# Kernel tuning notes

Measured on AMD Instinct MI355X. Metric: run time of the kernel, lower is better.

The kernel has to match this reference:

```python
import jax, jax.numpy as jnp
import numpy as np

# NF4 codebook (bitsandbytes quant_type='nf4'), 16 fixed quantile values
NF4 = jnp.array([
    -1.0, -0.6961928009986877, -0.5250730514526367, -0.39491748809814453,
    -0.28444138169288635, -0.18477343022823334, -0.09105003625154495, 0.0,
    0.07958029955625534, 0.16093020141124725, 0.24611230194568634,
    0.33791524171829224, 0.44070982933044434, 0.5626170039176941,
    0.7229568362236023, 1.0], dtype=jnp.float32)
BLK = 64  # bnb default blocksize for nf4


def dequant_nf4(codes, absmax):
    # codes: [out, in] int codes in [0,16); absmax: [out, in//BLK] blockwise scale
    out_f, in_f = codes.shape
    w = NF4[codes].reshape(out_f, in_f // BLK, BLK) * absmax[:, :, None]
    return w.reshape(out_f, in_f)


def setup_inputs() -> dict:
    key = jax.random.key(0)
    ks = jax.random.split(key, 7)
    hd, m, T = 4096, 14336, 2048
    x = jax.random.normal(ks[0], (T, hd), dtype=jnp.float32)
    gate_codes = jax.random.randint(ks[1], (m, hd), 0, 16, dtype=jnp.int32)
    gate_absmax = jax.random.uniform(ks[2], (m, hd // BLK), dtype=jnp.float32) * 0.05
    up_codes = jax.random.randint(ks[3], (m, hd), 0, 16, dtype=jnp.int32)
    up_absmax = jax.random.uniform(ks[4], (m, hd // BLK), dtype=jnp.float32) * 0.05
    down_codes = jax.random.randint(ks[5], (hd, m), 0, 16, dtype=jnp.int32)
    down_absmax = jax.random.uniform(ks[6], (hd, m // BLK), dtype=jnp.float32) * 0.05
    return {"x": x, "gate_codes": gate_codes, "gate_absmax": gate_absmax,
            "up_codes": up_codes, "up_absmax": up_absmax,
            "down_codes": down_codes, "down_absmax": down_absmax}


def reference(x, gate_codes, gate_absmax, up_codes, up_absmax, down_codes, down_absmax):
    # SwiGLU MLP: down( silu(gate(x)) * up(x) ), weights dequantized from nf4
    Wg = dequant_nf4(gate_codes, gate_absmax)   # [m, hd]
    Wu = dequant_nf4(up_codes, up_absmax)       # [m, hd]
    Wd = dequant_nf4(down_codes, down_absmax)   # [hd, m]
    g = x @ Wg.T                                # [T, m]
    h = jax.nn.silu(g) * (x @ Wu.T)             # [T, m]
    return h @ Wd.T                             # [T, hd]
```

## Files before the change

kernel.cpp:

```cpp
#include <hip/hip_runtime.h>
#include <hip/hip_bf16.h>
#include <cstdint>
#include <cstddef>

#define TDIM 2048
#define HDIM 4096
#define MDIM 14336

typedef __attribute__((ext_vector_type(8))) __bf16 bf16x8;
typedef __attribute__((ext_vector_type(4))) float f32x4;

__device__ __constant__ float NF4_LUT[16] = {
    -1.0f, -0.6961928009986877f, -0.5250730514526367f, -0.39491748809814453f,
    -0.28444138169288635f, -0.18477343022823334f, -0.09105003625154495f, 0.0f,
    0.07958029955625534f, 0.16093020141124725f, 0.24611230194568634f,
    0.33791524171829224f, 0.44070982933044434f, 0.5626170039176941f,
    0.7229568362236023f, 1.0f};

__device__ inline void g2l16(const void* g, void* l) {
  __builtin_amdgcn_global_load_lds(
      (const __attribute__((address_space(1))) unsigned int*)g,
      (__attribute__((address_space(3))) unsigned int*)l,
      16 , 0, 0);
}

__global__ __launch_bounds__(256) void f32_to_bf16_k(
    const float* __restrict__ in, __hip_bfloat16* __restrict__ out, int n8) {
  for (int i = blockIdx.x * 256 + threadIdx.x; i < n8; i += gridDim.x * 256) {
    const float4* p = (const float4*)(in + (size_t)i * 8);
    float4 a = p[0], b = p[1];
    union { __hip_bfloat16 h[8]; int4 v; } u;
    u.h[0] = __float2bfloat16(a.x);
    u.h[1] = __float2bfloat16(a.y);
    u.h[2] = __float2bfloat16(a.z);
    u.h[3] = __float2bfloat16(a.w);
    u.h[4] = __float2bfloat16(b.x);
    u.h[5] = __float2bfloat16(b.y);
    u.h[6] = __float2bfloat16(b.z);
    u.h[7] = __float2bfloat16(b.w);
    *(int4*)(out + (size_t)i * 8) = u.v;
  }
}

__global__ __launch_bounds__(256) void dequant_nf4_k(
    const int* __restrict__ codes, const float* __restrict__ absmax,
    __hip_bfloat16* __restrict__ W, int K) {
  __shared__ float lut[16];
  if (threadIdx.x < 16) lut[threadIdx.x] = NF4_LUT[threadIdx.x];
  __syncthreads();
  const int row = blockIdx.x;
  const int K8 = K >> 3;
  const size_t rbase = (size_t)row * K;
  for (int c8 = threadIdx.x; c8 < K8; c8 += 256) {
    const int col = c8 << 3;
    const float am = absmax[(size_t)row * (K >> 6) + (col >> 6)];
    const int4* cp = (const int4*)(codes + rbase + col);
    int4 ca = cp[0], cb = cp[1];
    union { __hip_bfloat16 h[8]; int4 v; } u;
    u.h[0] = __float2bfloat16(lut[ca.x & 15] * am);
    u.h[1] = __float2bfloat16(lut[ca.y & 15] * am);
    u.h[2] = __float2bfloat16(lut[ca.z & 15] * am);
    u.h[3] = __float2bfloat16(lut[ca.w & 15] * am);
    u.h[4] = __float2bfloat16(lut[cb.x & 15] * am);
    u.h[5] = __float2bfloat16(lut[cb.y & 15] * am);
    u.h[6] = __float2bfloat16(lut[cb.z & 15] * am);
    u.h[7] = __float2bfloat16(lut[cb.w & 15] * am);
    *(int4*)(W + rbase + col) = u.v;
  }
}

template <int EPI>
__global__ __launch_bounds__(256, 2) void gemm_nt_k(
    const __hip_bfloat16* __restrict__ A, const __hip_bfloat16* __restrict__ B,
    void* __restrict__ Cv, const __hip_bfloat16* __restrict__ Gin,
    int M, int N, int K) {
  __shared__ __align__(16) char sA[128 * 128];
  __shared__ __align__(16) char sB[128 * 128];

  const int tid = threadIdx.x;
  const int lane = tid & 63;
  const int wid = tid >> 6;

  const int nbn = N >> 7;
  const int nwg = (M >> 7) * nbn;
  const int cpx = nwg >> 3;
  const int bid = blockIdx.x;
  const int wg = (bid & 7) * cpx + (bid >> 3);
  const int bm = wg / nbn, bn = wg % nbn;

  const int srow = lane >> 3;
  const int scolb = ((lane & 7) ^ srow) << 4;
  const char* gA = (const char*)A +
      ((size_t)(bm * 128 + wid * 8 + srow) * K) * 2 + scolb;
  const char* gB = (const char*)B +
      ((size_t)(bn * 128 + wid * 8 + srow) * K) * 2 + scolb;
  const size_t cstep = (size_t)64 * K;
  char* lA = sA + wid * 1024;
  char* lB = sB + wid * 1024;

  const int wm = wid >> 1, wn = wid & 1;
  const int colsw = (((lane >> 4) << 4) ^ ((lane & 7) << 4));
  const int aoff = (wm * 64 + (lane & 15)) * 128 + colsw;
  const int boff = (wn * 64 + (lane & 15)) * 128 + colsw;

  f32x4 acc[4][4] = {};

  const int nk = K >> 6;
  for (int kt = 0; kt < nk; ++kt) {
    const char* pa = gA + (size_t)kt * 128;
    const char* pb = gB + (size_t)kt * 128;
#pragma unroll
    for (int c = 0; c < 4; ++c) {
      g2l16(pa + c * cstep, lA + c * 4096);
      g2l16(pb + c * cstep, lB + c * 4096);
    }
    __syncthreads();
#pragma unroll
    for (int ks = 0; ks < 2; ++ks) {
      bf16x8 af[4], bfr[4];
#pragma unroll
      for (int i = 0; i < 4; ++i) {
        af[i] = *(const bf16x8*)(sA + ((aoff + i * 2048) ^ (ks << 6)));
        bfr[i] = *(const bf16x8*)(sB + ((boff + i * 2048) ^ (ks << 6)));
      }
#pragma unroll
      for (int mi = 0; mi < 4; ++mi)
#pragma unroll
        for (int nj = 0; nj < 4; ++nj)
          acc[mi][nj] = __builtin_amdgcn_mfma_f32_16x16x32_bf16(
              af[mi], bfr[nj], acc[mi][nj], 0, 0, 0);
    }
    __syncthreads();
  }

  const int row0 = bm * 128 + wm * 64 + ((lane >> 4) << 2);
  const int col0 = bn * 128 + wn * 64 + (lane & 15);
#pragma unroll
  for (int mi = 0; mi < 4; ++mi) {
#pragma unroll
    for (int nj = 0; nj < 4; ++nj) {
#pragma unroll
      for (int r = 0; r < 4; ++r) {
        const size_t idx =
            (size_t)(row0 + mi * 16 + r) * N + (col0 + nj * 16);
        const float v = acc[mi][nj][r];
        if (EPI == 0) {
          ((__hip_bfloat16*)Cv)[idx] = __float2bfloat16(v);
        } else if (EPI == 1) {
          const float g = __bfloat162float(Gin[idx]);
          const float h = g / (1.0f + __expf(-g)) * v;
          ((__hip_bfloat16*)Cv)[idx] = __float2bfloat16(h);
        } else {
          ((float*)Cv)[idx] = v;
        }
      }
    }
  }
}

extern "C" void kernel_launch(void* const* d_in, const int* in_sizes, int n_in,
                              void* d_out, int out_size, void* d_ws,
                              size_t ws_size, hipStream_t stream) {
  const float* x = (const float*)d_in[0];
  const int* gate_codes = (const int*)d_in[1];
  const float* gate_absmax = (const float*)d_in[2];
  const int* up_codes = (const int*)d_in[3];
  const float* up_absmax = (const float*)d_in[4];
  const int* down_codes = (const int*)d_in[5];
  const float* down_absmax = (const float*)d_in[6];

  char* ws = (char*)d_ws;
  __hip_bfloat16* xb = (__hip_bfloat16*)ws;
  __hip_bfloat16* Wb =
      (__hip_bfloat16*)(ws + (size_t)TDIM * HDIM * 2);
  __hip_bfloat16* Hb =
      (__hip_bfloat16*)(ws + (size_t)TDIM * HDIM * 2 +
                        (size_t)MDIM * HDIM * 2);

  f32_to_bf16_k<<<2048, 256, 0, stream>>>(x, xb, (TDIM * HDIM) / 8);

  dequant_nf4_k<<<MDIM, 256, 0, stream>>>(gate_codes, gate_absmax, Wb, HDIM);
  gemm_nt_k<0><<<(TDIM / 128) * (MDIM / 128), 256, 0, stream>>>(
      xb, Wb, Hb, nullptr, TDIM, MDIM, HDIM);

  dequant_nf4_k<<<MDIM, 256, 0, stream>>>(up_codes, up_absmax, Wb, HDIM);
  gemm_nt_k<1><<<(TDIM / 128) * (MDIM / 128), 256, 0, stream>>>(
      xb, Wb, Hb, Hb, TDIM, MDIM, HDIM);

  dequant_nf4_k<<<HDIM, 256, 0, stream>>>(down_codes, down_absmax, Wb, MDIM);
  gemm_nt_k<2><<<(TDIM / 128) * (HDIM / 128), 256, 0, stream>>>(
      Hb, Wb, (float*)d_out, nullptr, TDIM, HDIM, MDIM);
}
```

Before: 1.061 ms.

## Fuse NF4 dequantization into GEMM B-tile loading and drop standalone dequant kernels

Removes the three separate dequant kernels and the bf16 weight buffer. Each GEMM workgroup now reads int32 NF4 codes and absmax directly, dequantizes them through a paired 256-entry float2 LUT in shared memory, and writes swizzled bf16 into the B tile. The next tile's codes are prefetched into registers during compute. The workgroup mapping is changed to be column-major over M tiles so that the tiles sharing weight rows run together, and the occupancy hint is raised to 3. This avoids writing and re-reading the dequantized weights, but adds ALU and register pressure inside the GEMM, and each of the 16 M-tiles re-reads the codes.

```diff
diff --git a/kernel.cpp b/kernel.cpp
--- a/kernel.cpp
+++ b/kernel.cpp
@@ -17,11 +17,10 @@
     0.33791524171829224f, 0.44070982933044434f, 0.5626170039176941f,
     0.7229568362236023f, 1.0f};
 
-__device__ inline void g2l16(const void* g, void* l) {
+__device__ __forceinline__ void g2l16(const void* g, void* l) {
   __builtin_amdgcn_global_load_lds(
       (const __attribute__((address_space(1))) unsigned int*)g,
-      (__attribute__((address_space(3))) unsigned int*)l,
-      16 , 0, 0);
+      (__attribute__((address_space(3))) unsigned int*)l, 16, 0, 0);
 }
 
 __global__ __launch_bounds__(256) void f32_to_bf16_k(
@@ -42,61 +41,44 @@
   }
 }
 
-__global__ __launch_bounds__(256) void dequant_nf4_k(
-    const int* __restrict__ codes, const float* __restrict__ absmax,
-    __hip_bfloat16* __restrict__ W, int K) {
-  __shared__ float lut[16];
-  if (threadIdx.x < 16) lut[threadIdx.x] = NF4_LUT[threadIdx.x];
-  __syncthreads();
-  const int row = blockIdx.x;
-  const int K8 = K >> 3;
-  const size_t rbase = (size_t)row * K;
-  for (int c8 = threadIdx.x; c8 < K8; c8 += 256) {
-    const int col = c8 << 3;
-    const float am = absmax[(size_t)row * (K >> 6) + (col >> 6)];
-    const int4* cp = (const int4*)(codes + rbase + col);
-    int4 ca = cp[0], cb = cp[1];
-    union { __hip_bfloat16 h[8]; int4 v; } u;
-    u.h[0] = __float2bfloat16(lut[ca.x & 15] * am);
-    u.h[1] = __float2bfloat16(lut[ca.y & 15] * am);
-    u.h[2] = __float2bfloat16(lut[ca.z & 15] * am);
-    u.h[3] = __float2bfloat16(lut[ca.w & 15] * am);
-    u.h[4] = __float2bfloat16(lut[cb.x & 15] * am);
-    u.h[5] = __float2bfloat16(lut[cb.y & 15] * am);
-    u.h[6] = __float2bfloat16(lut[cb.z & 15] * am);
-    u.h[7] = __float2bfloat16(lut[cb.w & 15] * am);
-    *(int4*)(W + rbase + col) = u.v;
-  }
-}
-
 template <int EPI>
-__global__ __launch_bounds__(256, 2) void gemm_nt_k(
-    const __hip_bfloat16* __restrict__ A, const __hip_bfloat16* __restrict__ B,
-    void* __restrict__ Cv, const __hip_bfloat16* __restrict__ Gin,
-    int M, int N, int K) {
+__global__ __launch_bounds__(256, 3) void gemm_fused_k(
+    const __hip_bfloat16* __restrict__ A, const int* __restrict__ Bc,
+    const float* __restrict__ Bam, void* __restrict__ Cv,
+    const __hip_bfloat16* __restrict__ Gin, int M, int N, int K) {
   __shared__ __align__(16) char sA[128 * 128];
   __shared__ __align__(16) char sB[128 * 128];
+  __shared__ float2 lut2[256];
 
   const int tid = threadIdx.x;
   const int lane = tid & 63;
   const int wid = tid >> 6;
 
+  lut2[tid] = make_float2(NF4_LUT[tid & 15], NF4_LUT[tid >> 4]);
+
+  const int nbm = M >> 7;
   const int nbn = N >> 7;
-  const int nwg = (M >> 7) * nbn;
-  const int cpx = nwg >> 3;
+  const int nwg = nbm * nbn;
+  const int q8 = nwg >> 3;
   const int bid = blockIdx.x;
-  const int wg = (bid & 7) * cpx + (bid >> 3);
-  const int bm = wg / nbn, bn = wg % nbn;
+  const int wg = (bid & 7) * q8 + (bid >> 3);
+  const int bn = wg / nbm;
+  const int bm = wg - bn * nbm;
 
   const int srow = lane >> 3;
   const int scolb = ((lane & 7) ^ srow) << 4;
   const char* gA = (const char*)A +
       ((size_t)(bm * 128 + wid * 8 + srow) * K) * 2 + scolb;
-  const char* gB = (const char*)B +
-      ((size_t)(bn * 128 + wid * 8 + srow) * K) * 2 + scolb;
   const size_t cstep = (size_t)64 * K;
   char* lA = sA + wid * 1024;
-  char* lB = sB + wid * 1024;
+
+  const int r = tid >> 1;
+  const int h = tid & 1;
+  const int Rrow = bn * 128 + r;
+  const int* cbase = Bc + (size_t)Rrow * K + h * 32;
+  const float* amrow = Bam + (size_t)Rrow * (K >> 6);
+  char* bwr = sB + r * 128;
+  const int rx = r & 7;
 
   const int wm = wid >> 1, wn = wid & 1;
   const int colsw = (((lane >> 4) << 4) ^ ((lane & 7) << 4));
@@ -105,30 +87,52 @@
 
   f32x4 acc[4][4] = {};
 
-  const int nk = K >> 6;
-  for (int kt = 0; kt < nk; ++kt) {
+  const int nt = K >> 6;
+  union { int w[32]; int4 v4[8]; } cw;
+#pragma unroll
+  for (int q = 0; q < 8; ++q) cw.v4[q] = ((const int4*)cbase)[q];
+  float am = amrow[0];
+
+  __syncthreads();
+
+  for (int kt = 0; kt < nt; ++kt) {
+#pragma unroll
+    for (int j = 0; j < 4; ++j) {
+      union { __hip_bfloat16 b[8]; int4 v; } ou;
+#pragma unroll
+      for (int p = 0; p < 4; ++p) {
+        const int w0 = cw.w[j * 8 + 2 * p];
+        const int w1 = cw.w[j * 8 + 2 * p + 1];
+        const float2 lv = lut2[(w0 & 15) | ((w1 & 15) << 4)];
+        ou.b[2 * p] = __float2bfloat16(lv.x * am);
+        ou.b[2 * p + 1] = __float2bfloat16(lv.y * am);
+      }
+      *(int4*)(bwr + ((((h << 2) | j) ^ rx) << 4)) = ou.v;
+    }
     const char* pa = gA + (size_t)kt * 128;
-    const char* pb = gB + (size_t)kt * 128;
 #pragma unroll
-    for (int c = 0; c < 4; ++c) {
-      g2l16(pa + c * cstep, lA + c * 4096);
-      g2l16(pb + c * cstep, lB + c * 4096);
+    for (int c = 0; c < 4; ++c) g2l16(pa + c * cstep, lA + c * 4096);
+    if (kt + 1 < nt) {
+      const int4* np = (const int4*)(cbase + (kt + 1) * 64);
+#pragma unroll
+      for (int q = 0; q < 8; ++q) cw.v4[q] = np[q];
+      am = amrow[kt + 1];
     }
     __syncthreads();
 #pragma unroll
     for (int ks = 0; ks < 2; ++ks) {
-      bf16x8 af[4], bfr[4];
+      bf16x8 af[4], bv[4];
 #pragma unroll
       for (int i = 0; i < 4; ++i) {
         af[i] = *(const bf16x8*)(sA + ((aoff + i * 2048) ^ (ks << 6)));
-        bfr[i] = *(const bf16x8*)(sB + ((boff + i * 2048) ^ (ks << 6)));
+        bv[i] = *(const bf16x8*)(sB + ((boff + i * 2048) ^ (ks << 6)));
       }
 #pragma unroll
       for (int mi = 0; mi < 4; ++mi)
 #pragma unroll
         for (int nj = 0; nj < 4; ++nj)
           acc[mi][nj] = __builtin_amdgcn_mfma_f32_16x16x32_bf16(
-              af[mi], bfr[nj], acc[mi][nj], 0, 0, 0);
+              af[mi], bv[nj], acc[mi][nj], 0, 0, 0);
     }
     __syncthreads();
   }
@@ -140,16 +144,16 @@
 #pragma unroll
     for (int nj = 0; nj < 4; ++nj) {
 #pragma unroll
-      for (int r = 0; r < 4; ++r) {
+      for (int rr = 0; rr < 4; ++rr) {
         const size_t idx =
-            (size_t)(row0 + mi * 16 + r) * N + (col0 + nj * 16);
-        const float v = acc[mi][nj][r];
+            (size_t)(row0 + mi * 16 + rr) * N + (col0 + nj * 16);
+        const float v = acc[mi][nj][rr];
         if (EPI == 0) {
           ((__hip_bfloat16*)Cv)[idx] = __float2bfloat16(v);
         } else if (EPI == 1) {
           const float g = __bfloat162float(Gin[idx]);
-          const float h = g / (1.0f + __expf(-g)) * v;
-          ((__hip_bfloat16*)Cv)[idx] = __float2bfloat16(h);
+          ((__hip_bfloat16*)Cv)[idx] =
+              __float2bfloat16(g / (1.0f + __expf(-g)) * v);
         } else {
           ((float*)Cv)[idx] = v;
         }
@@ -171,23 +175,14 @@
 
   char* ws = (char*)d_ws;
   __hip_bfloat16* xb = (__hip_bfloat16*)ws;
-  __hip_bfloat16* Wb =
-      (__hip_bfloat16*)(ws + (size_t)TDIM * HDIM * 2);
-  __hip_bfloat16* Hb =
-      (__hip_bfloat16*)(ws + (size_t)TDIM * HDIM * 2 +
-                        (size_t)MDIM * HDIM * 2);
+  __hip_bfloat16* Hb = (__hip_bfloat16*)(ws + (size_t)TDIM * HDIM * 2);
 
   f32_to_bf16_k<<<2048, 256, 0, stream>>>(x, xb, (TDIM * HDIM) / 8);
 
-  dequant_nf4_k<<<MDIM, 256, 0, stream>>>(gate_codes, gate_absmax, Wb, HDIM);
-  gemm_nt_k<0><<<(TDIM / 128) * (MDIM / 128), 256, 0, stream>>>(
-      xb, Wb, Hb, nullptr, TDIM, MDIM, HDIM);
-
-  dequant_nf4_k<<<MDIM, 256, 0, stream>>>(up_codes, up_absmax, Wb, HDIM);
-  gemm_nt_k<1><<<(TDIM / 128) * (MDIM / 128), 256, 0, stream>>>(
-      xb, Wb, Hb, Hb, TDIM, MDIM, HDIM);
-
-  dequant_nf4_k<<<HDIM, 256, 0, stream>>>(down_codes, down_absmax, Wb, MDIM);
-  gemm_nt_k<2><<<(TDIM / 128) * (HDIM / 128), 256, 0, stream>>>(
-      Hb, Wb, (float*)d_out, nullptr, TDIM, HDIM, MDIM);
+  gemm_fused_k<0><<<(TDIM / 128) * (MDIM / 128), 256, 0, stream>>>(
+      xb, gate_codes, gate_absmax, Hb, nullptr, TDIM, MDIM, HDIM);
+  gemm_fused_k<1><<<(TDIM / 128) * (MDIM / 128), 256, 0, stream>>>(
+      xb, up_codes, up_absmax, Hb, Hb, TDIM, MDIM, HDIM);
+  gemm_fused_k<2><<<(TDIM / 128) * (HDIM / 128), 256, 0, stream>>>(
+      Hb, down_codes, down_absmax, (float*)d_out, nullptr, TDIM, HDIM, MDIM);
 }
```

Result: slower. 2.012 ms (+89.6%).
